# Performance work log

Measured on AMD Instinct MI355X. Metric: run time of the kernel, lower is better.

Reference implementation:

```python
import jax, jax.numpy as jnp
import numpy as np

DIM_IN, DIM_H, NUM_CLASSES, TOPK = 384, 512, 2, 6
SCALE = DIM_H ** (-0.5)
LN_EPS = 1e-5


def setup_inputs() -> dict:
    key = jax.random.key(0)
    ks = jax.random.split(key, 16)
    p = lambda k, shape: jax.random.normal(k, shape, dtype=jnp.float32) * 0.02
    return {
        "feats": jax.random.normal(ks[0], (1, 8192, DIM_IN), dtype=jnp.float32),
        "fc1_w": p(ks[1], (DIM_IN, DIM_H)), "fc1_b": jnp.zeros((DIM_H,), jnp.float32),
        "wh_w": p(ks[2], (DIM_H, DIM_H)), "wh_b": jnp.zeros((DIM_H,), jnp.float32),
        "wt_w": p(ks[3], (DIM_H, DIM_H)), "wt_b": jnp.zeros((DIM_H,), jnp.float32),
        "l1_w": p(ks[4], (DIM_H, DIM_H)), "l1_b": jnp.zeros((DIM_H,), jnp.float32),
        "l2_w": p(ks[5], (DIM_H, DIM_H)), "l2_b": jnp.zeros((DIM_H,), jnp.float32),
        "ln_g": jnp.ones((DIM_H,), jnp.float32), "ln_b": jnp.zeros((DIM_H,), jnp.float32),
        "cls_w": p(ks[6], (DIM_H, NUM_CLASSES)), "cls_b": jnp.zeros((NUM_CLASSES,), jnp.float32),
    }


def _wikg_fwd(feats, fc1_w, fc1_b, wh_w, wh_b, wt_w, wt_b,
              l1_w, l1_b, l2_w, l2_b, ln_g, ln_b, cls_w, cls_b):
    lrelu = lambda v: jax.nn.leaky_relu(v, 0.01)
    x = lrelu(feats @ fc1_w + fc1_b)                      # [B,N,D]
    x = (x + x.mean(axis=1, keepdims=True)) * 0.5
    e_h = x @ wh_w + wh_b                                 # [B,N,D]
    e_t = x @ wt_w + wt_b                                 # [B,N,D]
    attn_logit = jnp.einsum('bnd,bmd->bnm', e_h * SCALE, e_t)  # [B,N,N]
    topk_weight, topk_index = jax.lax.top_k(attn_logit, TOPK)  # [B,N,K]
    # gather neighbor tail embeddings: Nb_h[b,n,k] = e_t[b, topk_index[b,n,k]]
    Nb_h = jax.vmap(lambda et, idx: et[idx])(e_t, topk_index)  # [B,N,K,D]
    topk_prob = jax.nn.softmax(topk_weight, axis=2)            # [B,N,K]
    eh_r = topk_prob[..., None] * Nb_h + (1.0 - topk_prob)[..., None] * e_h[:, :, None, :]
    gate = jnp.tanh(e_h[:, :, None, :] + eh_r)                 # [B,N,K,D]
    ka_weight = jnp.einsum('bnkd,bnkd->bnk', Nb_h, gate)       # [B,N,K]
    ka_prob = jax.nn.softmax(ka_weight, axis=2)
    e_Nh = jnp.einsum('bnk,bnkd->bnd', ka_prob, Nb_h)          # [B,N,D]
    # bi-interaction aggregation
    sum_emb = lrelu((e_h + e_Nh) @ l1_w + l1_b)
    bi_emb = lrelu((e_h * e_Nh) @ l2_w + l2_b)
    emb = sum_emb + bi_emb                                     # [B,N,D]
    # dropout is identity in eval mode; mean readout over nodes (B=1 squeezed)
    h = emb[0].mean(axis=0, keepdims=True)                     # [1,D]
    mu = h.mean(axis=-1, keepdims=True)
    var = ((h - mu) ** 2).mean(axis=-1, keepdims=True)
    h = (h - mu) * jax.lax.rsqrt(var + LN_EPS) * ln_g + ln_b
    return h @ cls_w + cls_b                                   # [1,num_classes]


def reference(feats, fc1_w, fc1_b, wh_w, wh_b, wt_w, wt_b,
              l1_w, l1_b, l2_w, l2_b, ln_g, ln_b, cls_w, cls_b):
    return _wikg_fwd(feats, fc1_w, fc1_b, wh_w, wh_b, wt_w, wt_b,
                     l1_w, l1_b, l2_w, l2_b, ln_g, ln_b, cls_w, cls_b)
```

## Files before the change

kernel.cpp:

```cpp
#include <hip/hip_runtime.h>
#include <math.h>

#define DEV __device__ __forceinline__

using frag_ab = __attribute__((ext_vector_type(8))) short;
using frag_cd = __attribute__((ext_vector_type(4))) float;

static constexpr float SCALE_C = 0.04419417382415922f;

DEV unsigned short f2bf(float f) {
    unsigned u = __float_as_uint(f);
    unsigned r = (u + 0x7FFFu + ((u >> 16) & 1u)) >> 16;
    return (unsigned short)r;
}
DEV float bf2f(unsigned short h) { return __uint_as_float(((unsigned)h) << 16); }

DEV void unpack8(uint4 q, float f[8]) {
    f[0] = bf2f((unsigned short)(q.x & 0xFFFFu)); f[1] = bf2f((unsigned short)(q.x >> 16));
    f[2] = bf2f((unsigned short)(q.y & 0xFFFFu)); f[3] = bf2f((unsigned short)(q.y >> 16));
    f[4] = bf2f((unsigned short)(q.z & 0xFFFFu)); f[5] = bf2f((unsigned short)(q.z >> 16));
    f[6] = bf2f((unsigned short)(q.w & 0xFFFFu)); f[7] = bf2f((unsigned short)(q.w >> 16));
}
DEV uint4 pack8(const float f[8]) {
    uint4 q;
    q.x = (unsigned)f2bf(f[0]) | ((unsigned)f2bf(f[1]) << 16);
    q.y = (unsigned)f2bf(f[2]) | ((unsigned)f2bf(f[3]) << 16);
    q.z = (unsigned)f2bf(f[4]) | ((unsigned)f2bf(f[5]) << 16);
    q.w = (unsigned)f2bf(f[6]) | ((unsigned)f2bf(f[7]) << 16);
    return q;
}

DEV unsigned mono(float f) {
    unsigned u = __float_as_uint(f);
    return u ^ ((unsigned)((int)u >> 31) | 0x80000000u);
}
DEV float unmono(unsigned k) {
    unsigned u = (k & 0x80000000u) ? (k & 0x7FFFFFFFu) : ~k;
    return __uint_as_float(u);
}

DEV void gload_lds16(const void* g, void* l) {
    __builtin_amdgcn_global_load_lds(
        (const __attribute__((address_space(1))) void*)g,
        (__attribute__((address_space(3))) void*)l, 16, 0, 0);
}

__global__ void k_prep(const float* __restrict__ feats, const float* __restrict__ fc1_w,
                       const float* __restrict__ wh_w, const float* __restrict__ wt_w,
                       const float* __restrict__ l1_w, const float* __restrict__ l2_w,
                       unsigned short* __restrict__ fb, unsigned short* __restrict__ wfc1T,
                       unsigned short* __restrict__ whT, unsigned short* __restrict__ wtT,
                       unsigned short* __restrict__ l1T, unsigned short* __restrict__ l2T) {
    const int z = blockIdx.z;
    if (z == 5) {
        for (int i = (blockIdx.x * 256 + threadIdx.x) * 4; i < 8192 * 384; i += 1024 * 256 * 4) {
            float4 v = *(const float4*)(feats + i);
            ushort4 o;
            o.x = f2bf(v.x); o.y = f2bf(v.y); o.z = f2bf(v.z); o.w = f2bf(v.w);
            *(ushort4*)(fb + i) = o;
        }
        return;
    }
    const float* s = z == 0 ? fc1_w : z == 1 ? wh_w : z == 2 ? wt_w : z == 3 ? l1_w : l2_w;
    unsigned short* d = z == 0 ? wfc1T : z == 1 ? whT : z == 2 ? wtT : z == 3 ? l1T : l2T;
    const int K = z == 0 ? 384 : 512;
    int i = blockIdx.x * 256 + threadIdx.x;
    if (i >= K * 512) return;
    int n = i / K, k = i - n * K;
    d[i] = f2bf(s[k * 512 + n]);
}

DEV void stage_async(const unsigned short* __restrict__ g, int ld, int k0, char* lds, int t) {
    const int sub = t >> 3;
    const int b = (t & 7) << 4;
    const int bs = b ^ ((sub & 7) << 4);
    const char* gb = (const char*)(g + k0) + (size_t)sub * (size_t)(ld * 2) + bs;
    char* lb = lds + ((t >> 6) << 10);
    const size_t rstep = (size_t)32 * (ld * 2);
#pragma unroll
    for (int r = 0; r < 4; ++r)
        gload_lds16(gb + r * rstep, lb + r * 4096);
}

DEV void mfma_tile(const char* As, const char* Bs, int lane, int wr, int wc, frag_cd (&acc)[4][4]) {
#pragma unroll
    for (int ks = 0; ks < 2; ++ks) {
        const int boff = ks * 64 + ((lane >> 4) << 4);
        frag_ab av[4];
#pragma unroll
        for (int f = 0; f < 4; ++f) {
            int ra = wr * 64 + f * 16 + (lane & 15);
            av[f] = *(const frag_ab*)(As + ra * 128 + (boff ^ ((ra & 7) << 4)));
        }
#pragma unroll
        for (int j = 0; j < 4; ++j) {
            int rb = wc * 64 + j * 16 + (lane & 15);
            frag_ab bv = *(const frag_ab*)(Bs + rb * 128 + (boff ^ ((rb & 7) << 4)));
#pragma unroll
            for (int i = 0; i < 4; ++i)
                acc[i][j] = __builtin_amdgcn_mfma_f32_16x16x32_bf16(av[i], bv, acc[i][j], 0, 0, 0);
        }
    }
}

DEV void mfma_tile_swp(const char* As, const char* Bs, int lane, int wr, int wc, frag_cd (&acc)[4][4]) {
#pragma unroll
    for (int ks = 0; ks < 2; ++ks) {
        const int boff = ks * 64 + ((lane >> 4) << 4);
        frag_ab av[4];
#pragma unroll
        for (int f = 0; f < 4; ++f) {
            int ra = wr * 64 + f * 16 + (lane & 15);
            av[f] = *(const frag_ab*)(As + ra * 128 + (boff ^ ((ra & 7) << 4)));
        }
#pragma unroll
        for (int j = 0; j < 4; ++j) {
            int rb = wc * 64 + j * 16 + (lane & 15);
            frag_ab bv = *(const frag_ab*)(Bs + rb * 128 + (boff ^ ((rb & 7) << 4)));
#pragma unroll
            for (int i = 0; i < 4; ++i)
                acc[i][j] = __builtin_amdgcn_mfma_f32_16x16x32_bf16(bv, av[i], acc[i][j], 0, 0, 0);
        }
    }
}

template <int ACT, int EPI>
__global__ __launch_bounds__(256, 2) void k_gemm(
    const unsigned short* __restrict__ A0, const unsigned short* __restrict__ A1,
    const unsigned short* __restrict__ B0, const unsigned short* __restrict__ B1,
    const float* __restrict__ bias0, const float* __restrict__ bias1,
    unsigned short* __restrict__ out0, unsigned short* __restrict__ out1,
    float* __restrict__ colsum, int M, int N, int K) {
    __shared__ __align__(16) char smem[65536];
    __shared__ float colacc[128];
    char* sA0 = smem;
    char* sA1 = smem + 16384;
    char* sB0 = smem + 32768;
    char* sB1 = smem + 49152;
    const int z = blockIdx.z;
    const unsigned short* A = z ? A1 : A0;
    const unsigned short* BT = z ? B1 : B0;
    const float* bias = z ? bias1 : bias0;
    unsigned short* out = z ? out1 : out0;
    const int t = threadIdx.x;
    const int lane = t & 63, wid = t >> 6, wr = wid >> 1, wc = wid & 1;
    const int m0 = blockIdx.x * 128, n0 = blockIdx.y * 128;
    if (EPI >= 1 && t < 128) colacc[t] = 0.f;
    const unsigned short* Ap = A + (size_t)m0 * K;
    const unsigned short* Bp = BT + (size_t)n0 * K;
    frag_cd acc[4][4] = {};
    const int nt = K >> 6;
    stage_async(Ap, K, 0, sA0, t);
    stage_async(Bp, K, 0, sB0, t);
    __syncthreads();
#pragma unroll 1
    for (int tt = 0; tt < nt - 2; tt += 2) {
        stage_async(Ap, K, (tt + 1) * 64, sA1, t);
        stage_async(Bp, K, (tt + 1) * 64, sB1, t);
        mfma_tile(sA0, sB0, lane, wr, wc, acc);
        __syncthreads();
        stage_async(Ap, K, (tt + 2) * 64, sA0, t);
        stage_async(Bp, K, (tt + 2) * 64, sB0, t);
        mfma_tile(sA1, sB1, lane, wr, wc, acc);
        __syncthreads();
    }
    stage_async(Ap, K, (nt - 1) * 64, sA1, t);
    stage_async(Bp, K, (nt - 1) * 64, sB1, t);
    mfma_tile(sA0, sB0, lane, wr, wc, acc);
    __syncthreads();
    mfma_tile(sA1, sB1, lane, wr, wc, acc);
    float bval[4];
#pragma unroll
    for (int j = 0; j < 4; ++j) bval[j] = bias[n0 + wc * 64 + j * 16 + (lane & 15)];
#pragma unroll
    for (int i = 0; i < 4; ++i) {
#pragma unroll
        for (int j = 0; j < 4; ++j) {
            float cs = 0.f;
#pragma unroll
            for (int r = 0; r < 4; ++r) {
                float v = acc[i][j][r] + bval[j];
                if (ACT) v = v > 0.f ? v : 0.01f * v;
                if (EPI != 2) {
                    int row = m0 + wr * 64 + i * 16 + (lane >> 4) * 4 + r;
                    int col = n0 + wc * 64 + j * 16 + (lane & 15);
                    out[(size_t)row * N + col] = f2bf(v);
                }
                cs += v;
            }
            if (EPI >= 1) atomicAdd(&colacc[wc * 64 + j * 16 + (lane & 15)], cs);
        }
    }
    if (EPI >= 1) {
        __syncthreads();
        if (t < 128) atomicAdd(&colsum[n0 + t], colacc[t]);
    }
}

__global__ void k_update_x(unsigned short* __restrict__ xb, const float* __restrict__ colsum) {
    int i = (blockIdx.x * 256 + threadIdx.x) * 8;
    uint4 q = *(const uint4*)(xb + i);
    float f[8]; unpack8(q, f);
    int c0 = i & 511;
#pragma unroll
    for (int j = 0; j < 8; ++j) f[j] = 0.5f * (f[j] + colsum[c0 + j] * (1.f / 8192.f));
    *(uint4*)(xb + i) = pack8(f);
}

DEV void kins(unsigned (&v)[6], unsigned k) {
    unsigned m1 = v[0] < k ? v[0] : k;
    unsigned m2 = v[1] < k ? v[1] : k;
    unsigned m3 = v[2] < k ? v[2] : k;
    unsigned m4 = v[3] < k ? v[3] : k;
    unsigned m5 = v[4] < k ? v[4] : k;
    v[0] = v[0] > k ? v[0] : k;
    v[1] = v[1] > m1 ? v[1] : m1;
    v[2] = v[2] > m2 ? v[2] : m2;
    v[3] = v[3] > m3 ? v[3] : m3;
    v[4] = v[4] > m4 ? v[4] : m4;
    v[5] = v[5] > m5 ? v[5] : m5;
}

__global__ __launch_bounds__(256, 2) void k_attn_topk(
    const unsigned short* __restrict__ ehb, const unsigned short* __restrict__ etb,
    unsigned* __restrict__ pk) {
    __shared__ __align__(16) char smem[65536];
    char* sA0 = smem;
    char* sA1 = smem + 16384;
    char* sB0 = smem + 32768;
    char* sB1 = smem + 49152;
    unsigned* xbuf = (unsigned*)smem;
    const int t = threadIdx.x;
    const int lane = t & 63, wid = t >> 6, wr = wid >> 1, wc = wid & 1;
    const int m0 = blockIdx.x * 128;
    const int csplit = blockIdx.y;
    const unsigned short* Ap = ehb + (size_t)m0 * 512;
    unsigned kl[4][6] = {};

    stage_async(Ap, 512, 0, sA0, t);
    stage_async(etb + (size_t)(csplit * 512) * 512, 512, 0, sB0, t);

#pragma unroll 1
    for (int ct = 0; ct < 4; ++ct) {
        const int n0 = csplit * 512 + ct * 128;
        const unsigned short* Bp = etb + (size_t)n0 * 512;
        frag_cd acc[4][4] = {};
        __syncthreads();
#pragma unroll 1
        for (int p = 0; p < 3; ++p) {
            stage_async(Ap, 512, (2 * p + 1) * 64, sA1, t);
            stage_async(Bp, 512, (2 * p + 1) * 64, sB1, t);
            mfma_tile_swp(sA0, sB0, lane, wr, wc, acc);
            __syncthreads();
            stage_async(Ap, 512, (2 * p + 2) * 64, sA0, t);
            stage_async(Bp, 512, (2 * p + 2) * 64, sB0, t);
            mfma_tile_swp(sA1, sB1, lane, wr, wc, acc);
            __syncthreads();
        }
        stage_async(Ap, 512, 7 * 64, sA1, t);
        stage_async(Bp, 512, 7 * 64, sB1, t);
        mfma_tile_swp(sA0, sB0, lane, wr, wc, acc);
        __syncthreads();
        if (ct < 3) {
            stage_async(Ap, 512, 0, sA0, t);
            stage_async(etb + (size_t)(n0 + 128) * 512, 512, 0, sB0, t);
        }
        mfma_tile_swp(sA1, sB1, lane, wr, wc, acc);
        const int base_ck = 8191 - (n0 + wc * 64 + ((lane >> 4) << 2));
#pragma unroll
        for (int i = 0; i < 4; ++i)
#pragma unroll
            for (int j = 0; j < 4; ++j)
#pragma unroll
                for (int r = 0; r < 4; ++r) {
                    unsigned key = (mono(acc[i][j][r]) & 0xFFFFE000u) |
                                   (unsigned)(base_ck - j * 16 - r);
                    kins(kl[i], key);
                }
    }
#pragma unroll
    for (int i = 0; i < 4; ++i) {
#pragma unroll
        for (int j = 0; j < 6; ++j) {
            unsigned ok = (unsigned)__shfl_xor((int)kl[i][j], 16, 64);
            kins(kl[i], ok);
        }
#pragma unroll
        for (int j = 0; j < 6; ++j) {
            unsigned ok = (unsigned)__shfl_xor((int)kl[i][j], 32, 64);
            kins(kl[i], ok);
        }
    }
    __syncthreads();
    if (wc == 1 && (lane >> 4) == 0) {
#pragma unroll
        for (int i = 0; i < 4; ++i) {
            int row = wr * 64 + i * 16 + lane;
#pragma unroll
            for (int j = 0; j < 6; ++j) xbuf[row * 6 + j] = kl[i][j];
        }
    }
    __syncthreads();
    if (wc == 0 && (lane >> 4) == 0) {
#pragma unroll
        for (int i = 0; i < 4; ++i) {
            int row = wr * 64 + i * 16 + lane;
#pragma unroll
            for (int j = 0; j < 6; ++j) kins(kl[i], xbuf[row * 6 + j]);
            size_t o = ((size_t)(m0 + row) * 16 + csplit) * 6;
#pragma unroll
            for (int j = 0; j < 6; ++j) pk[o + j] = kl[i][j];
        }
    }
}

__global__ void k_merge_topk(const unsigned* __restrict__ pk,
                             float* __restrict__ tw, int* __restrict__ ti) {
    int r = blockIdx.x * 256 + threadIdx.x;
    if (r >= 8192) return;
    unsigned v[6] = {0, 0, 0, 0, 0, 0};
    for (int s2 = 0; s2 < 16; ++s2) {
        const unsigned* p = pk + ((size_t)r * 16 + s2) * 6;
#pragma unroll
        for (int j = 0; j < 6; ++j) kins(v, p[j]);
    }
#pragma unroll
    for (int j = 0; j < 6; ++j) {
        tw[r * 6 + j] = unmono(v[j] & 0xFFFFE000u) * SCALE_C;
        ti[r * 6 + j] = 8191 - (int)(v[j] & 8191u);
    }
}

__global__ __launch_bounds__(256) void k_agg(
    const unsigned short* __restrict__ ehb, const unsigned short* __restrict__ etb,
    const float* __restrict__ tw, const int* __restrict__ ti,
    unsigned short* __restrict__ sb, unsigned short* __restrict__ pb) {
    const int t = threadIdx.x, lane = t & 63, wid = t >> 6;
    const int node = blockIdx.x * 4 + wid;
    const int d0 = lane * 8;
    float w[6]; int idx[6];
#pragma unroll
    for (int k = 0; k < 6; ++k) { w[k] = tw[node * 6 + k]; idx[k] = ti[node * 6 + k]; }
    float mx = w[0];
#pragma unroll
    for (int k = 1; k < 6; ++k) mx = fmaxf(mx, w[k]);
    float pr[6], s = 0.f;
#pragma unroll
    for (int k = 0; k < 6; ++k) { pr[k] = expf(w[k] - mx); s += pr[k]; }
    float inv = 1.f / s;
#pragma unroll
    for (int k = 0; k < 6; ++k) pr[k] *= inv;

    float eh[8]; unpack8(*(const uint4*)(ehb + (size_t)node * 512 + d0), eh);
    float nb[6][8];
#pragma unroll
    for (int k = 0; k < 6; ++k) unpack8(*(const uint4*)(etb + (size_t)idx[k] * 512 + d0), nb[k]);

    float kw[6] = {};
#pragma unroll
    for (int k = 0; k < 6; ++k) {
        float pk2 = pr[k];
#pragma unroll
        for (int j = 0; j < 8; ++j) {
            float ehr = pk2 * nb[k][j] + (1.f - pk2) * eh[j];
            float g = tanhf(eh[j] + ehr);
            kw[k] += nb[k][j] * g;
        }
    }
#pragma unroll
    for (int k = 0; k < 6; ++k)
#pragma unroll
        for (int o = 1; o < 64; o <<= 1) kw[k] += __shfl_xor(kw[k], o, 64);
    float m2 = kw[0];
#pragma unroll
    for (int k = 1; k < 6; ++k) m2 = fmaxf(m2, kw[k]);
    float kp[6], s2 = 0.f;
#pragma unroll
    for (int k = 0; k < 6; ++k) { kp[k] = expf(kw[k] - m2); s2 += kp[k]; }
    float inv2 = 1.f / s2;
#pragma unroll
    for (int k = 0; k < 6; ++k) kp[k] *= inv2;

    float sv[8], pv[8];
#pragma unroll
    for (int j = 0; j < 8; ++j) {
        float en = 0.f;
#pragma unroll
        for (int k = 0; k < 6; ++k) en += kp[k] * nb[k][j];
        sv[j] = eh[j] + en;
        pv[j] = eh[j] * en;
    }
    *(uint4*)(sb + (size_t)node * 512 + d0) = pack8(sv);
    *(uint4*)(pb + (size_t)node * 512 + d0) = pack8(pv);
}

DEV float blocksum512(float v, float* red, int lane, int wid) {
#pragma unroll
    for (int o = 1; o < 64; o <<= 1) v += __shfl_xor(v, o, 64);
    __syncthreads();
    if (lane == 0) red[wid] = v;
    __syncthreads();
    float s = 0.f;
#pragma unroll
    for (int w2 = 0; w2 < 8; ++w2) s += red[w2];
    return s;
}

__global__ __launch_bounds__(512) void k_final(
    const float* __restrict__ colsum_emb, const float* __restrict__ ln_g,
    const float* __restrict__ ln_b, const float* __restrict__ cls_w,
    const float* __restrict__ cls_b, float* __restrict__ out) {
    __shared__ float red[8];
    const int t = threadIdx.x, lane = t & 63, wid = t >> 6;
    float h = colsum_emb[t] * (1.f / 8192.f);
    float mu = blocksum512(h, red, lane, wid) * (1.f / 512.f);
    float d = h - mu;
    float var = blocksum512(d * d, red, lane, wid) * (1.f / 512.f);
    float y = d * rsqrtf(var + 1e-5f) * ln_g[t] + ln_b[t];
    float s0 = blocksum512(y * cls_w[t * 2 + 0], red, lane, wid);
    float s1 = blocksum512(y * cls_w[t * 2 + 1], red, lane, wid);
    if (t == 0) { out[0] = s0 + cls_b[0]; out[1] = s1 + cls_b[1]; }
}

extern "C" void kernel_launch(void* const* d_in, const int* in_sizes, int n_in,
                              void* d_out, int out_size, void* d_ws, size_t ws_size,
                              hipStream_t stream) {
    (void)in_sizes; (void)n_in; (void)out_size; (void)ws_size;
    const float* feats = (const float*)d_in[0];
    const float* fc1_w = (const float*)d_in[1];
    const float* fc1_b = (const float*)d_in[2];
    const float* wh_w  = (const float*)d_in[3];
    const float* wh_b  = (const float*)d_in[4];
    const float* wt_w  = (const float*)d_in[5];
    const float* wt_b  = (const float*)d_in[6];
    const float* l1_w  = (const float*)d_in[7];
    const float* l1_b  = (const float*)d_in[8];
    const float* l2_w  = (const float*)d_in[9];
    const float* l2_b  = (const float*)d_in[10];
    const float* ln_g  = (const float*)d_in[11];
    const float* ln_b  = (const float*)d_in[12];
    const float* cls_w = (const float*)d_in[13];
    const float* cls_b = (const float*)d_in[14];

    char* ws = (char*)d_ws;
    size_t off = 0;
    auto alloc = [&](size_t bytes) {
        char* p = ws + off;
        off += (bytes + 255) & ~(size_t)255;
        return p;
    };
    unsigned short* fb   = (unsigned short*)alloc(8192ull * 384 * 2);
    unsigned short* xb   = (unsigned short*)alloc(8192ull * 512 * 2);
    unsigned short* ehb  = (unsigned short*)alloc(8192ull * 512 * 2);
    unsigned short* etb  = (unsigned short*)alloc(8192ull * 512 * 2);
    unsigned short* sb   = (unsigned short*)alloc(8192ull * 512 * 2);
    unsigned short* pb   = (unsigned short*)alloc(8192ull * 512 * 2);
    unsigned short* wfc1T = (unsigned short*)alloc(512ull * 384 * 2);
    unsigned short* whT  = (unsigned short*)alloc(512ull * 512 * 2);
    unsigned short* wtT  = (unsigned short*)alloc(512ull * 512 * 2);
    unsigned short* l1T  = (unsigned short*)alloc(512ull * 512 * 2);
    unsigned short* l2T  = (unsigned short*)alloc(512ull * 512 * 2);
    float* colsum     = (float*)alloc(512 * 4);
    float* colsum_emb = (float*)alloc(512 * 4);
    unsigned* pk = (unsigned*)alloc(8192ull * 16 * 6 * 4);
    float* tw = (float*)alloc(8192ull * 6 * 4);
    int*   ti = (int*)alloc(8192ull * 6 * 4);

    hipMemsetAsync(colsum, 0, 512 * 4, stream);
    hipMemsetAsync(colsum_emb, 0, 512 * 4, stream);

    k_prep<<<dim3(1024, 1, 6), 256, 0, stream>>>(
        feats, fc1_w, wh_w, wt_w, l1_w, l2_w, fb, wfc1T, whT, wtT, l1T, l2T);

    k_gemm<1, 1><<<dim3(64, 4, 1), 256, 0, stream>>>(
        fb, fb, wfc1T, wfc1T, fc1_b, fc1_b, xb, xb, colsum, 8192, 512, 384);
    k_update_x<<<2048, 256, 0, stream>>>(xb, colsum);
    k_gemm<0, 0><<<dim3(64, 4, 2), 256, 0, stream>>>(
        xb, xb, whT, wtT, wh_b, wt_b, ehb, etb, nullptr, 8192, 512, 512);
    k_attn_topk<<<dim3(64, 16), 256, 0, stream>>>(ehb, etb, pk);
    k_merge_topk<<<32, 256, 0, stream>>>(pk, tw, ti);
    k_agg<<<2048, 256, 0, stream>>>(ehb, etb, tw, ti, sb, pb);
    k_gemm<1, 2><<<dim3(64, 4, 2), 256, 0, stream>>>(
        sb, pb, l1T, l2T, l1_b, l2_b, nullptr, nullptr, colsum_emb, 8192, 512, 512);
    k_final<<<1, 512, 0, stream>>>(colsum_emb, ln_g, ln_b, cls_w, cls_b, (float*)d_out);
}
```

Measured before the change: 182.7 us.

## Fold mean-update into projection bias, tile weight transpose, use med3 and fast tanh

```diff
diff --git a/kernel.cpp b/kernel.cpp
--- a/kernel.cpp
+++ b/kernel.cpp
@@ -52,8 +52,9 @@
                        unsigned short* __restrict__ whT, unsigned short* __restrict__ wtT,
                        unsigned short* __restrict__ l1T, unsigned short* __restrict__ l2T) {
     const int z = blockIdx.z;
+    const int tid = threadIdx.x;
     if (z == 5) {
-        for (int i = (blockIdx.x * 256 + threadIdx.x) * 4; i < 8192 * 384; i += 1024 * 256 * 4) {
+        for (int i = (blockIdx.x * 256 + tid) * 4; i < 8192 * 384; i += 256 * 256 * 4) {
             float4 v = *(const float4*)(feats + i);
             ushort4 o;
             o.x = f2bf(v.x); o.y = f2bf(v.y); o.z = f2bf(v.z); o.w = f2bf(v.w);
@@ -64,10 +65,47 @@
     const float* s = z == 0 ? fc1_w : z == 1 ? wh_w : z == 2 ? wt_w : z == 3 ? l1_w : l2_w;
     unsigned short* d = z == 0 ? wfc1T : z == 1 ? whT : z == 2 ? wtT : z == 3 ? l1T : l2T;
     const int K = z == 0 ? 384 : 512;
-    int i = blockIdx.x * 256 + threadIdx.x;
-    if (i >= K * 512) return;
-    int n = i / K, k = i - n * K;
-    d[i] = f2bf(s[k * 512 + n]);
+    const float scale = (z == 1 || z == 2) ? 0.5f : 1.0f;
+    const int ntk = K >> 6;
+    const int t = blockIdx.x;
+    if (t >= ntk * 8) return;
+    const int k0 = (t % ntk) * 64, n0 = (t / ntk) * 64;
+    __shared__ short tile[64 * 68];
+#pragma unroll
+    for (int p = 0; p < 4; ++p) {
+        int kk = p * 16 + (tid >> 4);
+        int nn = (tid & 15) * 4;
+        float4 v = *(const float4*)(s + (size_t)(k0 + kk) * 512 + n0 + nn);
+        tile[(nn + 0) * 68 + kk] = (short)f2bf(v.x * scale);
+        tile[(nn + 1) * 68 + kk] = (short)f2bf(v.y * scale);
+        tile[(nn + 2) * 68 + kk] = (short)f2bf(v.z * scale);
+        tile[(nn + 3) * 68 + kk] = (short)f2bf(v.w * scale);
+    }
+    __syncthreads();
+#pragma unroll
+    for (int p = 0; p < 2; ++p) {
+        int rr = p * 32 + (tid >> 3);
+        int cc = (tid & 7) * 8;
+        const short* rp = &tile[rr * 68 + cc];
+        uint2 a = *(const uint2*)(rp);
+        uint2 b = *(const uint2*)(rp + 4);
+        uint4 o = {a.x, a.y, b.x, b.y};
+        *(uint4*)(d + (size_t)(n0 + rr) * K + k0 + cc) = o;
+    }
+}
+
+__global__ __launch_bounds__(512) void k_rank1(
+    const float* __restrict__ colsum, const float* __restrict__ wh_w,
+    const float* __restrict__ wt_w, const float* __restrict__ wh_b,
+    const float* __restrict__ wt_b, float* __restrict__ cvh, float* __restrict__ cvt) {
+    const float* W = blockIdx.x ? wt_w : wh_w;
+    const float* b = blockIdx.x ? wt_b : wh_b;
+    float* cv = blockIdx.x ? cvt : cvh;
+    const int n = threadIdx.x;
+    float s = 0.f;
+#pragma unroll 8
+    for (int k = 0; k < 512; ++k) s += colsum[k] * W[k * 512 + n];
+    cv[n] = b[n] + s * (0.5f / 8192.f);
 }
 
 DEV void stage_async(const unsigned short* __restrict__ g, int ld, int k0, char* lds, int t) {
@@ -197,28 +235,19 @@
     }
 }
 
-__global__ void k_update_x(unsigned short* __restrict__ xb, const float* __restrict__ colsum) {
-    int i = (blockIdx.x * 256 + threadIdx.x) * 8;
-    uint4 q = *(const uint4*)(xb + i);
-    float f[8]; unpack8(q, f);
-    int c0 = i & 511;
-#pragma unroll
-    for (int j = 0; j < 8; ++j) f[j] = 0.5f * (f[j] + colsum[c0 + j] * (1.f / 8192.f));
-    *(uint4*)(xb + i) = pack8(f);
-}
-
+DEV unsigned med3u(unsigned a, unsigned b, unsigned c) {
+    unsigned r;
+    asm("v_med3_u32 %0, %1, %2, %3" : "=v"(r) : "v"(a), "v"(b), "v"(c));
+    return r;
+}
 DEV void kins(unsigned (&v)[6], unsigned k) {
-    unsigned m1 = v[0] < k ? v[0] : k;
-    unsigned m2 = v[1] < k ? v[1] : k;
-    unsigned m3 = v[2] < k ? v[2] : k;
-    unsigned m4 = v[3] < k ? v[3] : k;
-    unsigned m5 = v[4] < k ? v[4] : k;
+    unsigned t0 = v[0], t1 = v[1], t2 = v[2], t3 = v[3], t4 = v[4];
     v[0] = v[0] > k ? v[0] : k;
-    v[1] = v[1] > m1 ? v[1] : m1;
-    v[2] = v[2] > m2 ? v[2] : m2;
-    v[3] = v[3] > m3 ? v[3] : m3;
-    v[4] = v[4] > m4 ? v[4] : m4;
-    v[5] = v[5] > m5 ? v[5] : m5;
+    v[1] = med3u(t0, v[1], k);
+    v[2] = med3u(t1, v[2], k);
+    v[3] = med3u(t2, v[3], k);
+    v[4] = med3u(t3, v[4], k);
+    v[5] = med3u(t4, v[5], k);
 }
 
 __global__ __launch_bounds__(256, 2) void k_attn_topk(
@@ -250,22 +279,30 @@
         for (int p = 0; p < 3; ++p) {
             stage_async(Ap, 512, (2 * p + 1) * 64, sA1, t);
             stage_async(Bp, 512, (2 * p + 1) * 64, sB1, t);
+            __builtin_amdgcn_s_setprio(1);
             mfma_tile_swp(sA0, sB0, lane, wr, wc, acc);
+            __builtin_amdgcn_s_setprio(0);
             __syncthreads();
             stage_async(Ap, 512, (2 * p + 2) * 64, sA0, t);
             stage_async(Bp, 512, (2 * p + 2) * 64, sB0, t);
+            __builtin_amdgcn_s_setprio(1);
             mfma_tile_swp(sA1, sB1, lane, wr, wc, acc);
+            __builtin_amdgcn_s_setprio(0);
             __syncthreads();
         }
         stage_async(Ap, 512, 7 * 64, sA1, t);
         stage_async(Bp, 512, 7 * 64, sB1, t);
+        __builtin_amdgcn_s_setprio(1);
         mfma_tile_swp(sA0, sB0, lane, wr, wc, acc);
+        __builtin_amdgcn_s_setprio(0);
         __syncthreads();
         if (ct < 3) {
             stage_async(Ap, 512, 0, sA0, t);
             stage_async(etb + (size_t)(n0 + 128) * 512, 512, 0, sB0, t);
         }
+        __builtin_amdgcn_s_setprio(1);
         mfma_tile_swp(sA1, sB1, lane, wr, wc, acc);
+        __builtin_amdgcn_s_setprio(0);
         const int base_ck = 8191 - (n0 + wc * 64 + ((lane >> 4) << 2));
 #pragma unroll
         for (int i = 0; i < 4; ++i)
@@ -329,6 +366,11 @@
         tw[r * 6 + j] = unmono(v[j] & 0xFFFFE000u) * SCALE_C;
         ti[r * 6 + j] = 8191 - (int)(v[j] & 8191u);
     }
+}
+
+DEV float ftanh(float x) {
+    float t = __expf(2.f * x);
+    return 1.f - 2.f * __builtin_amdgcn_rcpf(t + 1.f);
 }
 
 __global__ __launch_bounds__(256) void k_agg(
@@ -346,7 +388,7 @@
     for (int k = 1; k < 6; ++k) mx = fmaxf(mx, w[k]);
     float pr[6], s = 0.f;
 #pragma unroll
-    for (int k = 0; k < 6; ++k) { pr[k] = expf(w[k] - mx); s += pr[k]; }
+    for (int k = 0; k < 6; ++k) { pr[k] = __expf(w[k] - mx); s += pr[k]; }
     float inv = 1.f / s;
 #pragma unroll
     for (int k = 0; k < 6; ++k) pr[k] *= inv;
@@ -363,7 +405,7 @@
 #pragma unroll
         for (int j = 0; j < 8; ++j) {
             float ehr = pk2 * nb[k][j] + (1.f - pk2) * eh[j];
-            float g = tanhf(eh[j] + ehr);
+            float g = ftanh(eh[j] + ehr);
             kw[k] += nb[k][j] * g;
         }
     }
@@ -376,7 +418,7 @@
     for (int k = 1; k < 6; ++k) m2 = fmaxf(m2, kw[k]);
     float kp[6], s2 = 0.f;
 #pragma unroll
-    for (int k = 0; k < 6; ++k) { kp[k] = expf(kw[k] - m2); s2 += kp[k]; }
+    for (int k = 0; k < 6; ++k) { kp[k] = __expf(kw[k] - m2); s2 += kp[k]; }
     float inv2 = 1.f / s2;
 #pragma unroll
     for (int k = 0; k < 6; ++k) kp[k] *= inv2;
@@ -462,6 +504,8 @@
     unsigned short* l2T  = (unsigned short*)alloc(512ull * 512 * 2);
     float* colsum     = (float*)alloc(512 * 4);
     float* colsum_emb = (float*)alloc(512 * 4);
+    float* cvh = (float*)alloc(512 * 4);
+    float* cvt = (float*)alloc(512 * 4);
     unsigned* pk = (unsigned*)alloc(8192ull * 16 * 6 * 4);
     float* tw = (float*)alloc(8192ull * 6 * 4);
     int*   ti = (int*)alloc(8192ull * 6 * 4);
@@ -469,14 +513,14 @@
     hipMemsetAsync(colsum, 0, 512 * 4, stream);
     hipMemsetAsync(colsum_emb, 0, 512 * 4, stream);
 
-    k_prep<<<dim3(1024, 1, 6), 256, 0, stream>>>(
+    k_prep<<<dim3(256, 1, 6), 256, 0, stream>>>(
         feats, fc1_w, wh_w, wt_w, l1_w, l2_w, fb, wfc1T, whT, wtT, l1T, l2T);
 
     k_gemm<1, 1><<<dim3(64, 4, 1), 256, 0, stream>>>(
         fb, fb, wfc1T, wfc1T, fc1_b, fc1_b, xb, xb, colsum, 8192, 512, 384);
-    k_update_x<<<2048, 256, 0, stream>>>(xb, colsum);
+    k_rank1<<<2, 512, 0, stream>>>(colsum, wh_w, wt_w, wh_b, wt_b, cvh, cvt);
     k_gemm<0, 0><<<dim3(64, 4, 2), 256, 0, stream>>>(
-        xb, xb, whT, wtT, wh_b, wt_b, ehb, etb, nullptr, 8192, 512, 512);
+        xb, xb, whT, wtT, cvh, cvt, ehb, etb, nullptr, 8192, 512, 512);
     k_attn_topk<<<dim3(64, 16), 256, 0, stream>>>(ehb, etb, pk);
     k_merge_topk<<<32, 256, 0, stream>>>(pk, tw, ti);
     k_agg<<<2048, 256, 0, stream>>>(ehb, etb, tw, ti, sb, pb);
```

Measured after the change: 191.3 us. 4.7% more time.
